# Optimization experiments

Measured on AMD Instinct MI355X. Metric: run time of the kernel, lower is better.

Reference implementation:

```python
import jax, jax.numpy as jnp
import numpy as np

N = 50000       # nodes
E = 800000      # edges (before self-loops)
F_IN = 128      # per-head input features (nfeat * t_size, t_size=1)
NHID = 128
NHEADS = 4
NCLASS = 64
NEG_SLOPE = 0.2   # GATConv leakyrelu negative_slope
ALPHA = 0.2       # outer LeakyReLU(alpha)


def setup_inputs():
    key = jax.random.key(0)
    ks = jax.random.split(key, 10)
    type_emb = jax.random.normal(ks[0], (NHEADS, N, F_IN), jnp.float32)
    edge = jax.random.randint(ks[1], (2, E), 0, N, dtype=jnp.int32)
    W = jax.random.normal(ks[2], (NHEADS, F_IN, NHID), jnp.float32) / np.sqrt(F_IN).astype(np.float32)
    att_src = jax.random.normal(ks[3], (NHEADS, NHID), jnp.float32) * 0.1
    att_dst = jax.random.normal(ks[4], (NHEADS, NHID), jnp.float32) * 0.1
    bias = jnp.zeros((NHEADS, NHID), jnp.float32)
    W_out = jax.random.normal(ks[5], (NHID * NHEADS, NCLASS), jnp.float32) / np.sqrt(NHID * NHEADS).astype(np.float32)
    att_src_out = jax.random.normal(ks[6], (NCLASS,), jnp.float32) * 0.1
    att_dst_out = jax.random.normal(ks[7], (NCLASS,), jnp.float32) * 0.1
    bias_out = jnp.zeros((NCLASS,), jnp.float32)
    return {"type_emb": type_emb, "edge": edge, "W": W, "att_src": att_src,
            "att_dst": att_dst, "bias": bias, "W_out": W_out,
            "att_src_out": att_src_out, "att_dst_out": att_dst_out,
            "bias_out": bias_out}


def _gat_conv(x, src, dst, W, a_src, a_dst, b):
    """PyG GATConv, heads=1, with self-loops already in (src, dst)."""
    xs = x @ W                                      # [N, H]
    e = jax.nn.leaky_relu((xs @ a_src)[src] + (xs @ a_dst)[dst], NEG_SLOPE)  # [E']
    # segment softmax over destination nodes (every node has a self-loop -> no empty segment)
    m = jax.ops.segment_max(e, dst, num_segments=N)
    ex = jnp.exp(e - m[dst])
    denom = jax.ops.segment_sum(ex, dst, num_segments=N)
    alpha = ex / denom[dst]                          # [E']
    out = jax.ops.segment_sum(alpha[:, None] * xs[src], dst, num_segments=N)  # [N, H]
    return out + b


def reference(type_emb, edge, W, att_src, att_dst, bias, W_out,
              att_src_out, att_dst_out, bias_out):
    loop = jnp.arange(N, dtype=edge.dtype)
    src = jnp.concatenate([edge[0], loop])
    dst = jnp.concatenate([edge[1], loop])
    # per-head GraphAttentionLayer: GATConv -> LeakyReLU(alpha) (dropout inactive)
    heads = [jax.nn.leaky_relu(
                 _gat_conv(type_emb[i], src, dst, W[i], att_src[i], att_dst[i], bias[i]),
                 ALPHA)
             for i in range(NHEADS)]
    x = jnp.concatenate(heads, axis=1)               # [N, NHID*NHEADS]
    y = jax.nn.leaky_relu(
            _gat_conv(x, src, dst, W_out, att_src_out, att_dst_out, bias_out),
            ALPHA)
    return jnp.tanh(y)                               # [N, NCLASS]
```

## Files before the change

kernel.cpp:

```cpp
#include <hip/hip_runtime.h>
#include <cmath>

#define NN 50000
#define EE 800000
#define ETOT (EE + NN)
#define NSCAN ((NN + 1023) / 1024)

typedef __bf16 v8bf __attribute__((ext_vector_type(8)));
typedef float f32x4 __attribute__((ext_vector_type(4)));

__device__ __forceinline__ float lrelu(float x){ return x > 0.0f ? x : 0.2f * x; }
__device__ __forceinline__ int bcast_i(int v, int j){ return __builtin_amdgcn_readlane(v, j); }
__device__ __forceinline__ float bcast_f(float v, int j){
  return __uint_as_float(__builtin_amdgcn_readlane(__float_as_uint(v), j));
}
__device__ __forceinline__ unsigned short f2bf_rne(float x){
  unsigned int u = __float_as_uint(x);
  u += 0x7fffu + ((u >> 16) & 1u);
  return (unsigned short)(u >> 16);
}
__device__ __forceinline__ float bf2f(unsigned short b){
  return __uint_as_float(((unsigned int)b) << 16);
}

__global__ void k_hist(const int* __restrict__ dst, int* __restrict__ cnt){
  int i = blockIdx.x * 256 + threadIdx.x;
  if (i >= ETOT) return;
  int d = (i < EE) ? dst[i] : (i - EE);
  atomicAdd(&cnt[d], 1);
}

__global__ void k_scan1(const int* __restrict__ cnt, int* __restrict__ part){
  __shared__ int sm[256];
  int b = blockIdx.x, t = threadIdx.x;
  int base = b * 1024 + t * 4;
  int s = 0;
  #pragma unroll
  for (int j = 0; j < 4; j++) if (base + j < NN) s += cnt[base + j];
  sm[t] = s; __syncthreads();
  for (int off = 128; off; off >>= 1){
    if (t < off) sm[t] += sm[t + off];
    __syncthreads();
  }
  if (t == 0) part[b] = sm[0];
}

__global__ void k_scan2(const int* __restrict__ part, int* __restrict__ part2){
  if (threadIdx.x == 0 && blockIdx.x == 0){
    int run = 0;
    for (int i = 0; i < NSCAN; i++){ part2[i] = run; run += part[i]; }
  }
}

__global__ void k_scan3(const int* __restrict__ cnt, const int* __restrict__ part2,
                        int* __restrict__ rowptr){
  __shared__ int sm[256];
  int b = blockIdx.x, t = threadIdx.x;
  int base = b * 1024 + t * 4;
  int v[4]; int s = 0;
  #pragma unroll
  for (int j = 0; j < 4; j++){ v[j] = (base + j < NN) ? cnt[base + j] : 0; s += v[j]; }
  sm[t] = s; __syncthreads();
  for (int off = 1; off < 256; off <<= 1){
    int x = (t >= off) ? sm[t - off] : 0;
    __syncthreads();
    sm[t] += x;
    __syncthreads();
  }
  int run = part2[b] + sm[t] - s;
  #pragma unroll
  for (int j = 0; j < 4; j++){
    if (base + j < NN){ rowptr[base + j] = run; run += v[j]; }
  }
  if (b == 0 && t == 0) rowptr[NN] = ETOT;
}

__global__ void k_scatter(const int* __restrict__ src, const int* __restrict__ dst,
                          const int* __restrict__ rowptr, int* __restrict__ fill,
                          int* __restrict__ csr){
  int i = blockIdx.x * 256 + threadIdx.x;
  if (i >= ETOT) return;
  int s, d;
  if (i < EE){ s = src[i]; d = dst[i]; } else { s = d = i - EE; }
  int pos = rowptr[d] + atomicAdd(&fill[d], 1);
  csr[pos] = s;
}

__global__ void k_convB(const float* __restrict__ B, unsigned short* __restrict__ bh,
                        unsigned short* __restrict__ bl, int K, int N, int total){
  int i = blockIdx.x * 256 + threadIdx.x;
  if (i >= total) return;
  int per = K * N;
  int h = i / per, rem = i - h * per;
  int k = rem / N, n = rem - k * N;
  float x = B[i];
  unsigned short hb = f2bf_rne(x);
  unsigned short lb = f2bf_rne(x - bf2f(hb));
  size_t o = (size_t)h * per + ((size_t)(k >> 3) * N + n) * 8 + (k & 7);
  bh[o] = hb; bl[o] = lb;
}

template<int BN, int OSTR, int SSTR>
__global__ __launch_bounds__(256) void gemm_split(const float* __restrict__ A,
                                                  const unsigned short* __restrict__ Bh,
                                                  const unsigned short* __restrict__ Bl,
                                                  unsigned short* __restrict__ out,
                                                  int M, int K,
                                                  const float* __restrict__ att_s,
                                                  const float* __restrict__ att_d,
                                                  float* __restrict__ ssrc,
                                                  float* __restrict__ sdst){
  const int t = threadIdx.x;
  const int wv = t >> 6, lane = t & 63;
  const int m0 = blockIdx.x * 128;
  const int h = blockIdx.y;
  A  += (size_t)h * M * K;
  Bh += (size_t)h * (K >> 3) * BN * 8;
  Bl += (size_t)h * (K >> 3) * BN * 8;
  const int colOff = h * BN;

  __shared__ v8bf sAh[4][128];
  __shared__ v8bf sAl[4][128];
  __shared__ v8bf sBh[4][BN];
  __shared__ v8bf sBl[4][BN];

  f32x4 acc[2][BN / 16];
  #pragma unroll
  for (int i = 0; i < 2; i++)
    #pragma unroll
    for (int j = 0; j < BN / 16; j++){
      f32x4 z = {0.f, 0.f, 0.f, 0.f};
      acc[i][j] = z;
    }

  const int mRow = t & 127;
  const int kh = (t >> 7) * 16;
  const bool valid = (m0 + mRow) < M;
  const int q = lane >> 4, lm = lane & 15;

  for (int k0 = 0; k0 < K; k0 += 32){
    const float* ap = A + (size_t)(m0 + mRow) * K + k0 + kh;
    float4 v0, v1, v2, v3;
    if (valid){
      v0 = *(const float4*)(ap);
      v1 = *(const float4*)(ap + 4);
      v2 = *(const float4*)(ap + 8);
      v3 = *(const float4*)(ap + 12);
    } else {
      v0 = v1 = v2 = v3 = make_float4(0.f, 0.f, 0.f, 0.f);
    }
    #pragma unroll
    for (int g = 0; g < 2; g++){
      float xv[8];
      if (g == 0){ xv[0]=v0.x; xv[1]=v0.y; xv[2]=v0.z; xv[3]=v0.w; xv[4]=v1.x; xv[5]=v1.y; xv[6]=v1.z; xv[7]=v1.w; }
      else       { xv[0]=v2.x; xv[1]=v2.y; xv[2]=v2.z; xv[3]=v2.w; xv[4]=v3.x; xv[5]=v3.y; xv[6]=v3.z; xv[7]=v3.w; }
      union { v8bf v; unsigned short u[8]; } H, L;
      #pragma unroll
      for (int i = 0; i < 8; i++){
        unsigned short hb = f2bf_rne(xv[i]);
        H.u[i] = hb;
        L.u[i] = f2bf_rne(xv[i] - bf2f(hb));
      }
      int k8 = (kh >> 3) + g;
      sAh[k8][mRow] = H.v;
      sAl[k8][mRow] = L.v;
    }
    {
      const v8bf* gh = (const v8bf*)Bh + (size_t)(k0 >> 3) * BN;
      const v8bf* gl = (const v8bf*)Bl + (size_t)(k0 >> 3) * BN;
      v8bf* dh = &sBh[0][0];
      v8bf* dl = &sBl[0][0];
      #pragma unroll
      for (int i = t; i < 4 * BN; i += 256){ dh[i] = gh[i]; dl[i] = gl[i]; }
    }
    __syncthreads();
    v8bf ah[2], al[2];
    #pragma unroll
    for (int rt = 0; rt < 2; rt++){
      int m = wv * 32 + rt * 16 + lm;
      ah[rt] = sAh[q][m];
      al[rt] = sAl[q][m];
    }
    #pragma unroll
    for (int ct = 0; ct < BN / 16; ct++){
      v8bf bh = sBh[q][ct * 16 + lm];
      v8bf bl = sBl[q][ct * 16 + lm];
      #pragma unroll
      for (int rt = 0; rt < 2; rt++){
        acc[rt][ct] = __builtin_amdgcn_mfma_f32_16x16x32_bf16(ah[rt], bh, acc[rt][ct], 0, 0, 0);
        acc[rt][ct] = __builtin_amdgcn_mfma_f32_16x16x32_bf16(ah[rt], bl, acc[rt][ct], 0, 0, 0);
        acc[rt][ct] = __builtin_amdgcn_mfma_f32_16x16x32_bf16(al[rt], bh, acc[rt][ct], 0, 0, 0);
      }
    }
    __syncthreads();
  }

  float asv[BN / 16], adv[BN / 16];
  #pragma unroll
  for (int ct = 0; ct < BN / 16; ct++){
    asv[ct] = att_s[h * BN + ct * 16 + lm];
    adv[ct] = att_d[h * BN + ct * 16 + lm];
  }

  #pragma unroll
  for (int rt = 0; rt < 2; rt++){
    #pragma unroll
    for (int reg = 0; reg < 4; reg++){
      int r = m0 + wv * 32 + rt * 16 + q * 4 + reg;
      float d0 = 0.f, d1 = 0.f;
      #pragma unroll
      for (int ct = 0; ct < BN / 16; ct++){
        float v = acc[rt][ct][reg];
        d0 += v * asv[ct];
        d1 += v * adv[ct];
      }
      #pragma unroll
      for (int off = 1; off < 16; off <<= 1){
        d0 += __shfl_xor(d0, off, 64);
        d1 += __shfl_xor(d1, off, 64);
      }
      if (r < M){
        unsigned short* orow = out + (size_t)r * OSTR + colOff + lm;
        #pragma unroll
        for (int ct = 0; ct < BN / 16; ct++)
          orow[ct * 16] = f2bf_rne(acc[rt][ct][reg]);
        if (lm == 0){
          ssrc[(size_t)r * SSTR + h] = d0;
          sdst[(size_t)r * SSTR + h] = d1;
        }
      }
    }
  }
}

__global__ __launch_bounds__(256) void k_agg4(const int* __restrict__ rowptr,
                                              const int* __restrict__ csr,
                                              const float* __restrict__ ssrc,
                                              const float* __restrict__ sdst,
                                              const unsigned short* __restrict__ xs_all,
                                              const float* __restrict__ bias,
                                              float* __restrict__ x1){
  int n = (blockIdx.x * 256 + threadIdx.x) >> 6;
  int lane = threadIdx.x & 63;
  if (n >= NN) return;
  int start = rowptr[n], end = rowptr[n + 1];
  float4 sd = ((const float4*)sdst)[n];
  int myh = lane >> 4;

  float s0 = 0.f, s1 = 0.f, s2 = 0.f, s3 = 0.f;
  float acc[8];
  #pragma unroll
  for (int i = 0; i < 8; i++) acc[i] = 0.f;

  for (int cb = start; cb < end; cb += 64){
    int e = cb + lane;
    int sl = 0; float w0 = 0.f, w1 = 0.f, w2 = 0.f, w3 = 0.f;
    if (e < end){
      sl = csr[e];
      float4 sv = ((const float4*)ssrc)[sl];
      w0 = __expf(lrelu(sv.x + sd.x));
      w1 = __expf(lrelu(sv.y + sd.y));
      w2 = __expf(lrelu(sv.z + sd.z));
      w3 = __expf(lrelu(sv.w + sd.w));
      s0 += w0; s1 += w1; s2 += w2; s3 += w3;
    }
    int cnt = min(64, end - cb);
    for (int j = 0; j < cnt; j++){
      int s = bcast_i(sl, j);
      float wa = bcast_f(w0, j), wb = bcast_f(w1, j);
      float wc = bcast_f(w2, j), wd = bcast_f(w3, j);
      float wm = (myh == 0) ? wa : (myh == 1) ? wb : (myh == 2) ? wc : wd;
      uint4 u = ((const uint4*)xs_all)[(size_t)s * 64 + lane];
      acc[0] += wm * __uint_as_float(u.x << 16);
      acc[1] += wm * __uint_as_float(u.x & 0xffff0000u);
      acc[2] += wm * __uint_as_float(u.y << 16);
      acc[3] += wm * __uint_as_float(u.y & 0xffff0000u);
      acc[4] += wm * __uint_as_float(u.z << 16);
      acc[5] += wm * __uint_as_float(u.z & 0xffff0000u);
      acc[6] += wm * __uint_as_float(u.w << 16);
      acc[7] += wm * __uint_as_float(u.w & 0xffff0000u);
    }
  }

  #pragma unroll
  for (int off = 32; off; off >>= 1){
    s0 += __shfl_xor(s0, off, 64);
    s1 += __shfl_xor(s1, off, 64);
    s2 += __shfl_xor(s2, off, 64);
    s3 += __shfl_xor(s3, off, 64);
  }
  float inv = 1.f / ((myh == 0) ? s0 : (myh == 1) ? s1 : (myh == 2) ? s2 : s3);

  const float* bp = bias + lane * 8;
  float4 bb0 = *(const float4*)bp, bb1 = *(const float4*)(bp + 4);
  float o[8];
  o[0] = lrelu(acc[0] * inv + bb0.x); o[1] = lrelu(acc[1] * inv + bb0.y);
  o[2] = lrelu(acc[2] * inv + bb0.z); o[3] = lrelu(acc[3] * inv + bb0.w);
  o[4] = lrelu(acc[4] * inv + bb1.x); o[5] = lrelu(acc[5] * inv + bb1.y);
  o[6] = lrelu(acc[6] * inv + bb1.z); o[7] = lrelu(acc[7] * inv + bb1.w);
  float* op = x1 + (size_t)n * 512 + lane * 8;
  *(float4*)op       = make_float4(o[0], o[1], o[2], o[3]);
  *(float4*)(op + 4) = make_float4(o[4], o[5], o[6], o[7]);
}

__global__ __launch_bounds__(256) void k_agg2(const int* __restrict__ rowptr,
                                              const int* __restrict__ csr,
                                              const float* __restrict__ ssrc,
                                              const float* __restrict__ sdst,
                                              const unsigned short* __restrict__ xs2,
                                              const float* __restrict__ bias,
                                              float* __restrict__ outp){
  int n = (blockIdx.x * 256 + threadIdx.x) >> 6;
  int lane = threadIdx.x & 63;
  if (n >= NN) return;
  int start = rowptr[n], end = rowptr[n + 1];
  float sdn = sdst[n];

  int half = lane >> 5, sub = lane & 31;
  float sloc = 0.f, acc0 = 0.f, acc1 = 0.f;
  for (int cb = start; cb < end; cb += 64){
    int e = cb + lane;
    int sl = 0; float w = 0.f;
    if (e < end){
      sl = csr[e];
      w = __expf(lrelu(ssrc[sl] + sdn));
      sloc += w;
    }
    int cnt = min(64, end - cb);
    for (int jj = 0; jj * 2 < cnt; jj++){
      int j0 = jj * 2, j1 = jj * 2 + 1;
      int sa = bcast_i(sl, j0); float wa = bcast_f(w, j0);
      int sb = bcast_i(sl, j1); float wb = bcast_f(w, j1);
      int ss = half ? sb : sa;
      float ws = half ? wb : wa;
      unsigned int u = ((const unsigned int*)xs2)[(size_t)ss * 32 + sub];
      acc0 += ws * __uint_as_float(u << 16);
      acc1 += ws * __uint_as_float(u & 0xffff0000u);
    }
  }
  #pragma unroll
  for (int off = 32; off; off >>= 1) sloc += __shfl_xor(sloc, off, 64);
  float inv = 1.f / sloc;

  acc0 += __shfl_xor(acc0, 32, 64);
  acc1 += __shfl_xor(acc1, 32, 64);
  if (lane < 32){
    float o0 = tanhf(lrelu(acc0 * inv + bias[sub * 2]));
    float o1 = tanhf(lrelu(acc1 * inv + bias[sub * 2 + 1]));
    *(float2*)(outp + (size_t)n * 64 + sub * 2) = make_float2(o0, o1);
  }
}

extern "C" void kernel_launch(void* const* d_in, const int* in_sizes, int n_in,
                              void* d_out, int out_size, void* d_ws, size_t ws_size,
                              hipStream_t stream){
  const float* type_emb  = (const float*)d_in[0];
  const int*   edge      = (const int*)d_in[1];
  const float* W         = (const float*)d_in[2];
  const float* att_src   = (const float*)d_in[3];
  const float* att_dst   = (const float*)d_in[4];
  const float* bias      = (const float*)d_in[5];
  const float* W_out     = (const float*)d_in[6];
  const float* att_src_o = (const float*)d_in[7];
  const float* att_dst_o = (const float*)d_in[8];
  const float* bias_o    = (const float*)d_in[9];
  float* out = (float*)d_out;
  (void)in_sizes; (void)n_in; (void)out_size; (void)ws_size;

  char* ws = (char*)d_ws;
  size_t off = 0;
  auto alloc = [&](size_t bytes) -> void* {
    void* p = ws + off;
    off = (off + bytes + 255) & ~(size_t)255;
    return p;
  };
  unsigned short* xs_all = (unsigned short*)alloc((size_t)NN * 512 * 2);
  float*          x1     = (float*)alloc((size_t)NN * 512 * 4);
  unsigned short* xs2    = (unsigned short*)alloc((size_t)NN * 64 * 2);
  float* ssrc1 = (float*)alloc((size_t)NN * 4 * 4);
  float* sdst1 = (float*)alloc((size_t)NN * 4 * 4);
  float* ssrc2 = (float*)alloc((size_t)NN * 4);
  float* sdst2 = (float*)alloc((size_t)NN * 4);
  int* cnt    = (int*)alloc((size_t)NN * 4);
  int* rowptr = (int*)alloc((size_t)(NN + 1) * 4);
  int* fill   = (int*)alloc((size_t)NN * 4);
  int* csr    = (int*)alloc((size_t)ETOT * 4);
  int* p1     = (int*)alloc((size_t)NSCAN * 4 + 256);
  int* p2     = (int*)alloc((size_t)NSCAN * 4 + 256);
  unsigned short* Bh1 = (unsigned short*)alloc((size_t)4 * 128 * 128 * 2);
  unsigned short* Bl1 = (unsigned short*)alloc((size_t)4 * 128 * 128 * 2);
  unsigned short* Bh2 = (unsigned short*)alloc((size_t)512 * 64 * 2);
  unsigned short* Bl2 = (unsigned short*)alloc((size_t)512 * 64 * 2);

  hipMemsetAsync(cnt, 0, (size_t)NN * 4, stream);
  hipMemsetAsync(fill, 0, (size_t)NN * 4, stream);
  k_hist<<<(ETOT + 255) / 256, 256, 0, stream>>>(edge + EE, cnt);
  k_scan1<<<NSCAN, 256, 0, stream>>>(cnt, p1);
  k_scan2<<<1, 64, 0, stream>>>(p1, p2);
  k_scan3<<<NSCAN, 256, 0, stream>>>(cnt, p2, rowptr);
  k_scatter<<<(ETOT + 255) / 256, 256, 0, stream>>>(edge, edge + EE, rowptr, fill, csr);

  k_convB<<<(4 * 128 * 128 + 255) / 256, 256, 0, stream>>>(W, Bh1, Bl1, 128, 128, 4 * 128 * 128);
  k_convB<<<(512 * 64 + 255) / 256, 256, 0, stream>>>(W_out, Bh2, Bl2, 512, 64, 512 * 64);

  gemm_split<128, 512, 4><<<dim3(391, 4), 256, 0, stream>>>(
      type_emb, Bh1, Bl1, xs_all, NN, 128, att_src, att_dst, ssrc1, sdst1);
  k_agg4<<<12500, 256, 0, stream>>>(rowptr, csr, ssrc1, sdst1, xs_all, bias, x1);

  gemm_split<64, 64, 1><<<dim3(391, 1), 256, 0, stream>>>(
      x1, Bh2, Bl2, xs2, NN, 512, att_src_o, att_dst_o, ssrc2, sdst2);
  k_agg2<<<12500, 256, 0, stream>>>(rowptr, csr, ssrc2, sdst2, xs2, bias_o, out);
}
```

Measured before the change: 499.3 us.

## Split layer-1 aggregation per head and process multiple edges per wavefront

The first aggregation kernel now launches one wavefront per (node, head) pair instead of one per node. Within the wavefront, four 16-lane groups each take a different edge and do 16-byte loads of that head's features, then reduce across groups with shuffles. The second aggregation kernel also moves from 2 edges per step with 4-byte loads to 8 edges per step with 16-byte loads. The aim is more memory-level parallelism and fewer serial edge iterations, at the cost of redundant CSR and softmax-weight work per head and extra cross-lane reductions.

```diff
diff --git a/kernel.cpp b/kernel.cpp
--- a/kernel.cpp
+++ b/kernel.cpp
@@ -10,10 +10,6 @@
 typedef float f32x4 __attribute__((ext_vector_type(4)));
 
 __device__ __forceinline__ float lrelu(float x){ return x > 0.0f ? x : 0.2f * x; }
-__device__ __forceinline__ int bcast_i(int v, int j){ return __builtin_amdgcn_readlane(v, j); }
-__device__ __forceinline__ float bcast_f(float v, int j){
-  return __uint_as_float(__builtin_amdgcn_readlane(__float_as_uint(v), j));
-}
 __device__ __forceinline__ unsigned short f2bf_rne(float x){
   unsigned int u = __float_as_uint(x);
   u += 0x7fffu + ((u >> 16) & 1u);
@@ -233,7 +229,7 @@
   }
 }
 
-__global__ __launch_bounds__(256) void k_agg4(const int* __restrict__ rowptr,
+__global__ __launch_bounds__(256) void k_agg1(const int* __restrict__ rowptr,
                                               const int* __restrict__ csr,
                                               const float* __restrict__ ssrc,
                                               const float* __restrict__ sdst,
@@ -241,66 +237,65 @@
                                               const float* __restrict__ bias,
                                               float* __restrict__ x1){
   int n = (blockIdx.x * 256 + threadIdx.x) >> 6;
+  int h = blockIdx.y;
   int lane = threadIdx.x & 63;
   if (n >= NN) return;
   int start = rowptr[n], end = rowptr[n + 1];
-  float4 sd = ((const float4*)sdst)[n];
-  int myh = lane >> 4;
-
-  float s0 = 0.f, s1 = 0.f, s2 = 0.f, s3 = 0.f;
+  float sdn = sdst[(size_t)n * 4 + h];
+  int g = lane >> 4, lm = lane & 15;
+
+  float sloc = 0.f;
   float acc[8];
   #pragma unroll
   for (int i = 0; i < 8; i++) acc[i] = 0.f;
 
   for (int cb = start; cb < end; cb += 64){
     int e = cb + lane;
-    int sl = 0; float w0 = 0.f, w1 = 0.f, w2 = 0.f, w3 = 0.f;
+    int sl = 0; float w = 0.f;
     if (e < end){
       sl = csr[e];
-      float4 sv = ((const float4*)ssrc)[sl];
-      w0 = __expf(lrelu(sv.x + sd.x));
-      w1 = __expf(lrelu(sv.y + sd.y));
-      w2 = __expf(lrelu(sv.z + sd.z));
-      w3 = __expf(lrelu(sv.w + sd.w));
-      s0 += w0; s1 += w1; s2 += w2; s3 += w3;
+      w = __expf(lrelu(ssrc[(size_t)sl * 4 + h] + sdn));
+      sloc += w;
     }
     int cnt = min(64, end - cb);
-    for (int j = 0; j < cnt; j++){
-      int s = bcast_i(sl, j);
-      float wa = bcast_f(w0, j), wb = bcast_f(w1, j);
-      float wc = bcast_f(w2, j), wd = bcast_f(w3, j);
-      float wm = (myh == 0) ? wa : (myh == 1) ? wb : (myh == 2) ? wc : wd;
-      uint4 u = ((const uint4*)xs_all)[(size_t)s * 64 + lane];
-      acc[0] += wm * __uint_as_float(u.x << 16);
-      acc[1] += wm * __uint_as_float(u.x & 0xffff0000u);
-      acc[2] += wm * __uint_as_float(u.y << 16);
-      acc[3] += wm * __uint_as_float(u.y & 0xffff0000u);
-      acc[4] += wm * __uint_as_float(u.z << 16);
-      acc[5] += wm * __uint_as_float(u.z & 0xffff0000u);
-      acc[6] += wm * __uint_as_float(u.w << 16);
-      acc[7] += wm * __uint_as_float(u.w & 0xffff0000u);
-    }
-  }
-
-  #pragma unroll
-  for (int off = 32; off; off >>= 1){
-    s0 += __shfl_xor(s0, off, 64);
-    s1 += __shfl_xor(s1, off, 64);
-    s2 += __shfl_xor(s2, off, 64);
-    s3 += __shfl_xor(s3, off, 64);
-  }
-  float inv = 1.f / ((myh == 0) ? s0 : (myh == 1) ? s1 : (myh == 2) ? s2 : s3);
-
-  const float* bp = bias + lane * 8;
-  float4 bb0 = *(const float4*)bp, bb1 = *(const float4*)(bp + 4);
-  float o[8];
-  o[0] = lrelu(acc[0] * inv + bb0.x); o[1] = lrelu(acc[1] * inv + bb0.y);
-  o[2] = lrelu(acc[2] * inv + bb0.z); o[3] = lrelu(acc[3] * inv + bb0.w);
-  o[4] = lrelu(acc[4] * inv + bb1.x); o[5] = lrelu(acc[5] * inv + bb1.y);
-  o[6] = lrelu(acc[6] * inv + bb1.z); o[7] = lrelu(acc[7] * inv + bb1.w);
-  float* op = x1 + (size_t)n * 512 + lane * 8;
-  *(float4*)op       = make_float4(o[0], o[1], o[2], o[3]);
-  *(float4*)(op + 4) = make_float4(o[4], o[5], o[6], o[7]);
+    for (int jj = 0; jj * 4 < cnt; jj++){
+      int j = jj * 4 + g;
+      int s = __shfl(sl, j, 64);
+      float ws = __shfl(w, j, 64);
+      uint4 u = ((const uint4*)xs_all)[(size_t)s * 64 + h * 16 + lm];
+      acc[0] += ws * __uint_as_float(u.x << 16);
+      acc[1] += ws * __uint_as_float(u.x & 0xffff0000u);
+      acc[2] += ws * __uint_as_float(u.y << 16);
+      acc[3] += ws * __uint_as_float(u.y & 0xffff0000u);
+      acc[4] += ws * __uint_as_float(u.z << 16);
+      acc[5] += ws * __uint_as_float(u.z & 0xffff0000u);
+      acc[6] += ws * __uint_as_float(u.w << 16);
+      acc[7] += ws * __uint_as_float(u.w & 0xffff0000u);
+    }
+  }
+
+  #pragma unroll
+  for (int off = 32; off; off >>= 1) sloc += __shfl_xor(sloc, off, 64);
+  float inv = 1.f / sloc;
+
+  #pragma unroll
+  for (int i = 0; i < 8; i++){
+    acc[i] += __shfl_xor(acc[i], 16, 64);
+    acc[i] += __shfl_xor(acc[i], 32, 64);
+  }
+
+  if (g == 0){
+    const float* bp = bias + h * 128 + lm * 8;
+    float4 b0 = *(const float4*)bp, b1 = *(const float4*)(bp + 4);
+    float o[8];
+    o[0] = lrelu(acc[0] * inv + b0.x); o[1] = lrelu(acc[1] * inv + b0.y);
+    o[2] = lrelu(acc[2] * inv + b0.z); o[3] = lrelu(acc[3] * inv + b0.w);
+    o[4] = lrelu(acc[4] * inv + b1.x); o[5] = lrelu(acc[5] * inv + b1.y);
+    o[6] = lrelu(acc[6] * inv + b1.z); o[7] = lrelu(acc[7] * inv + b1.w);
+    float* op = x1 + (size_t)n * 512 + h * 128 + lm * 8;
+    *(float4*)op       = make_float4(o[0], o[1], o[2], o[3]);
+    *(float4*)(op + 4) = make_float4(o[4], o[5], o[6], o[7]);
+  }
 }
 
 __global__ __launch_bounds__(256) void k_agg2(const int* __restrict__ rowptr,
@@ -315,9 +310,13 @@
   if (n >= NN) return;
   int start = rowptr[n], end = rowptr[n + 1];
   float sdn = sdst[n];
-
-  int half = lane >> 5, sub = lane & 31;
-  float sloc = 0.f, acc0 = 0.f, acc1 = 0.f;
+  int g = lane >> 3, lm = lane & 7;
+
+  float sloc = 0.f;
+  float acc[8];
+  #pragma unroll
+  for (int i = 0; i < 8; i++) acc[i] = 0.f;
+
   for (int cb = start; cb < end; cb += 64){
     int e = cb + lane;
     int sl = 0; float w = 0.f;
@@ -327,27 +326,41 @@
       sloc += w;
     }
     int cnt = min(64, end - cb);
-    for (int jj = 0; jj * 2 < cnt; jj++){
-      int j0 = jj * 2, j1 = jj * 2 + 1;
-      int sa = bcast_i(sl, j0); float wa = bcast_f(w, j0);
-      int sb = bcast_i(sl, j1); float wb = bcast_f(w, j1);
-      int ss = half ? sb : sa;
-      float ws = half ? wb : wa;
-      unsigned int u = ((const unsigned int*)xs2)[(size_t)ss * 32 + sub];
-      acc0 += ws * __uint_as_float(u << 16);
-      acc1 += ws * __uint_as_float(u & 0xffff0000u);
-    }
-  }
+    for (int jj = 0; jj * 8 < cnt; jj++){
+      int j = jj * 8 + g;
+      int s = __shfl(sl, j, 64);
+      float ws = __shfl(w, j, 64);
+      uint4 u = ((const uint4*)xs2)[(size_t)s * 8 + lm];
+      acc[0] += ws * __uint_as_float(u.x << 16);
+      acc[1] += ws * __uint_as_float(u.x & 0xffff0000u);
+      acc[2] += ws * __uint_as_float(u.y << 16);
+      acc[3] += ws * __uint_as_float(u.y & 0xffff0000u);
+      acc[4] += ws * __uint_as_float(u.z << 16);
+      acc[5] += ws * __uint_as_float(u.z & 0xffff0000u);
+      acc[6] += ws * __uint_as_float(u.w << 16);
+      acc[7] += ws * __uint_as_float(u.w & 0xffff0000u);
+    }
+  }
+
   #pragma unroll
   for (int off = 32; off; off >>= 1) sloc += __shfl_xor(sloc, off, 64);
   float inv = 1.f / sloc;
 
-  acc0 += __shfl_xor(acc0, 32, 64);
-  acc1 += __shfl_xor(acc1, 32, 64);
-  if (lane < 32){
-    float o0 = tanhf(lrelu(acc0 * inv + bias[sub * 2]));
-    float o1 = tanhf(lrelu(acc1 * inv + bias[sub * 2 + 1]));
-    *(float2*)(outp + (size_t)n * 64 + sub * 2) = make_float2(o0, o1);
+  #pragma unroll
+  for (int i = 0; i < 8; i++){
+    acc[i] += __shfl_xor(acc[i], 8, 64);
+    acc[i] += __shfl_xor(acc[i], 16, 64);
+    acc[i] += __shfl_xor(acc[i], 32, 64);
+  }
+
+  if (g == 0){
+    float o[8];
+    #pragma unroll
+    for (int i = 0; i < 8; i++)
+      o[i] = tanhf(lrelu(acc[i] * inv + bias[lm * 8 + i]));
+    float* op = outp + (size_t)n * 64 + lm * 8;
+    *(float4*)op       = make_float4(o[0], o[1], o[2], o[3]);
+    *(float4*)(op + 4) = make_float4(o[4], o[5], o[6], o[7]);
   }
 }
 
@@ -405,7 +418,7 @@
 
   gemm_split<128, 512, 4><<<dim3(391, 4), 256, 0, stream>>>(
       type_emb, Bh1, Bl1, xs_all, NN, 128, att_src, att_dst, ssrc1, sdst1);
-  k_agg4<<<12500, 256, 0, stream>>>(rowptr, csr, ssrc1, sdst1, xs_all, bias, x1);
+  k_agg1<<<dim3(12500, 4), 256, 0, stream>>>(rowptr, csr, ssrc1, sdst1, xs_all, bias, x1);
 
   gemm_split<64, 64, 1><<<dim3(391, 1), 256, 0, stream>>>(
       x1, Bh2, Bl2, xs2, NN, 512, att_src_o, att_dst_o, ssrc2, sdst2);
```

New measurement: 491.1 us. Within noise of the previous version (-1.6%).
